# Performance work log

Hardware: AMD Instinct MI355X
Metric: run time of the kernel (lower is better)

The kernel has to match this reference:

```python
import jax, jax.numpy as jnp
import numpy as np

D_MODEL = 1024
D_FF = 2048
N_EXPERTS = 4
TOP_K = 2
INIT_STD = 0.02


def setup_inputs() -> dict:
    key = jax.random.key(0)
    ks = jax.random.split(key, 5)
    hidden_states = jax.random.normal(ks[0], (2, 2048, D_MODEL), dtype=jnp.float32)
    # gate: nn.Linear(d_model, num_experts, bias=False) -> weight [E, D]
    w_gate = jax.random.normal(ks[1], (N_EXPERTS, D_MODEL), dtype=jnp.float32) * INIT_STD
    # per-expert GLU MLP weights, stacked over the expert axis
    w_gate_proj = jax.random.normal(ks[2], (N_EXPERTS, D_MODEL, D_FF), dtype=jnp.float32) * INIT_STD
    w_up_proj = jax.random.normal(ks[3], (N_EXPERTS, D_MODEL, D_FF), dtype=jnp.float32) * INIT_STD
    w_down_proj = jax.random.normal(ks[4], (N_EXPERTS, D_FF, D_MODEL), dtype=jnp.float32) * INIT_STD
    return {
        "hidden_states": hidden_states,
        "w_gate": w_gate,
        "w_gate_proj": w_gate_proj,
        "w_up_proj": w_up_proj,
        "w_down_proj": w_down_proj,
    }


def reference(hidden_states, w_gate, w_gate_proj, w_up_proj, w_down_proj):
    B, S, D = hidden_states.shape
    x = hidden_states.reshape(-1, D)  # [T, D]
    # --- routing ---
    router_logits = x @ w_gate.T  # [T, E]
    routing_probs = jax.nn.softmax(router_logits.astype(jnp.float32), axis=-1)
    topw, sel = jax.lax.top_k(routing_probs, TOP_K)  # [T, K]
    topw = topw / jnp.sum(topw, axis=-1, keepdims=True)  # norm_topk_prob=True
    topw = topw.astype(x.dtype)
    # combine weights per (token, expert): zero for non-selected experts
    cw = jnp.sum(jax.nn.one_hot(sel, N_EXPERTS, dtype=x.dtype) * topw[..., None], axis=1)  # [T, E]
    # --- expert GLU MLPs (dense over experts, masked combine) ---
    g = jnp.einsum('td,edf->etf', x, w_gate_proj)  # [E, T, F]
    u = jnp.einsum('td,edf->etf', x, w_up_proj)
    h = jax.nn.gelu(g, approximate=False) * u  # torch F.gelu default = exact erf
    y = jnp.einsum('etf,efd->etd', h, w_down_proj)  # [E, T, D]
    out = jnp.einsum('etd,te->td', y, cw)  # weighted scatter-combine
    # dropout p=0.0 (eval) -> identity
    return out.reshape(B, S, D)
```

## Files before the change

### kernel.cpp

```cpp
#include <hip/hip_runtime.h>
#include <hip/hip_bf16.h>
#include <math.h>


typedef float  f32x4 __attribute__((ext_vector_type(4)));
typedef short  s16x8 __attribute__((ext_vector_type(8)));

__device__ __forceinline__ unsigned short f2bf(float f) {
  union { float f; unsigned int u; } v; v.f = f;
  return (unsigned short)((v.u + 0x7fffu + ((v.u >> 16) & 1u)) >> 16);
}

__device__ __forceinline__ void glds16(const void* g, void* l) {
  __builtin_amdgcn_global_load_lds(
      (const __attribute__((address_space(1))) void*)g,
      (__attribute__((address_space(3))) void*)l, 16, 0, 0);
}

__global__ void k_routing(const float* __restrict__ x, const float* __restrict__ wg,
                          float* __restrict__ cw, int* __restrict__ idx,
                          int* __restrict__ cnt, unsigned short* __restrict__ Xb) {
  const int lane = threadIdx.x & 63;
  const int tok  = blockIdx.x * 4 + (threadIdx.x >> 6);
  const float4* X4 = (const float4*)x + (size_t)tok * 256;
  const float4* W4 = (const float4*)wg;
  ushort4* O4 = (ushort4*)Xb + (size_t)tok * 256;
  float a0 = 0.f, a1 = 0.f, a2 = 0.f, a3 = 0.f;
#pragma unroll
  for (int j = 0; j < 4; ++j) {
    const int d4 = j * 64 + lane;
    const float4 v = X4[d4];
    ushort4 o;
    o.x = f2bf(v.x); o.y = f2bf(v.y); o.z = f2bf(v.z); o.w = f2bf(v.w);
    O4[d4] = o;
    float4 w;
    w = W4[0 * 256 + d4]; a0 += v.x * w.x + v.y * w.y + v.z * w.z + v.w * w.w;
    w = W4[1 * 256 + d4]; a1 += v.x * w.x + v.y * w.y + v.z * w.z + v.w * w.w;
    w = W4[2 * 256 + d4]; a2 += v.x * w.x + v.y * w.y + v.z * w.z + v.w * w.w;
    w = W4[3 * 256 + d4]; a3 += v.x * w.x + v.y * w.y + v.z * w.z + v.w * w.w;
  }
#pragma unroll
  for (int off = 32; off; off >>= 1) {
    a0 += __shfl_xor(a0, off);
    a1 += __shfl_xor(a1, off);
    a2 += __shfl_xor(a2, off);
    a3 += __shfl_xor(a3, off);
  }
  if (lane == 0) {
    float l[4] = {a0, a1, a2, a3};
    const float m = fmaxf(fmaxf(l[0], l[1]), fmaxf(l[2], l[3]));
    float p[4];
#pragma unroll
    for (int e = 0; e < 4; ++e) p[e] = expf(l[e] - m);
    int i1 = 0; float b1 = p[0];
#pragma unroll
    for (int e = 1; e < 4; ++e) if (p[e] > b1) { b1 = p[e]; i1 = e; }
    int i2 = -1; float b2 = -1.f;
#pragma unroll
    for (int e = 0; e < 4; ++e) if (e != i1 && p[e] > b2) { b2 = p[e]; i2 = e; }
    const float inv = 1.f / (b1 + b2);
    float o[4] = {0.f, 0.f, 0.f, 0.f};
    o[i1] = b1 * inv; o[i2] = b2 * inv;
    *(float4*)(cw + (size_t)tok * 4) = make_float4(o[0], o[1], o[2], o[3]);
    const int p1 = atomicAdd(&cnt[i1], 1); idx[i1 * 4096 + p1] = tok;
    const int p2 = atomicAdd(&cnt[i2], 1); idx[i2 * 4096 + p2] = tok;
  }
}

__global__ void k_offsets(const int* __restrict__ cnt, int* __restrict__ off) {
  if (threadIdx.x == 0 && blockIdx.x == 0) {
    int o = 0, q = 0, p = 0;
#pragma unroll
    for (int e = 0; e < 4; ++e) {
      off[e] = o; off[4 + e] = q; off[9 + e] = p;
      o += (cnt[e] + 255) & ~255;
      q += (cnt[e] + 255) >> 8;
      p += (cnt[e] + 127) >> 7;
    }
    off[8] = q; off[13] = p;
  }
}

__global__ void k_tcvt_all(const float* __restrict__ wgp, const float* __restrict__ wup,
                           const float* __restrict__ wdp,
                           unsigned short* __restrict__ Wcat,
                           unsigned short* __restrict__ Wdt) {
  __shared__ float t[64][65];
  const int z = blockIdx.z;
  const int tx = threadIdx.x, ty = threadIdx.y;
  const float* in; unsigned short* outp; int R, C, c0, r0, cat = 0, addup = 0;
  if (z < 8) {
    R = 1024; C = 2048;
    const int e = z & 3;
    in   = (z < 4 ? wgp : wup) + (size_t)e * 1024 * 2048;
    outp = Wcat + (size_t)e * 4096 * 1024;
    c0 = blockIdx.x * 64; r0 = blockIdx.y * 64;
    cat = 1; addup = (z >= 4) ? 16 : 0;
  } else {
    R = 2048; C = 1024;
    const int e = z & 3;
    in   = wdp + (size_t)e * 2048 * 1024;
    outp = Wdt + (size_t)e * 2048 * 1024;
    c0 = blockIdx.y * 64; r0 = blockIdx.x * 64;
  }
#pragma unroll
  for (int i = 0; i < 16; ++i) {
    const int r = i * 4 + ty;
    t[r][tx] = in[(size_t)(r0 + r) * C + c0 + tx];
  }
  __syncthreads();
#pragma unroll
  for (int i = 0; i < 16; ++i) {
    const int cc = i * 4 + ty;
    const int f = c0 + cc;
    const int orow = cat ? (((f >> 4) << 5) + (f & 15) + addup) : f;
    outp[(size_t)orow * R + r0 + tx] = f2bf(t[tx][cc]);
  }
}

__global__ __launch_bounds__(512, 2)
void k_gemm1(const unsigned short* __restrict__ Xb,
             const unsigned short* __restrict__ Wcat,
             unsigned short* __restrict__ H,
             const int* __restrict__ idx, const int* __restrict__ cnt,
             const int* __restrict__ off) {
  const int w0 = (blockIdx.x & 7) * 72 + (blockIdx.x >> 3);
  const int bn = w0 / 36, mt = w0 % 36;
  const int* t1 = off + 4;
  if (mt >= t1[4]) return;
  const int e = (mt >= t1[1]) + (mt >= t1[2]) + (mt >= t1[3]);
  const int local = mt - t1[e];
  const int cn = cnt[e];
  const int lr0 = local * 256;
  const int hrow0 = off[e] + lr0;

  __shared__ __align__(16) unsigned short lds[2][2][256 * 64];

  const int tid = threadIdx.x;
  const int lane = tid & 63, wv = tid >> 6;
  const int wm = wv >> 2, wn = wv & 3;
  const int l15 = lane & 15;
  const int kb0 = ((lane >> 4) * 16) ^ ((lane & 7) << 4);
  const int kb1 = kb0 ^ 64;
  const int lrow = lane >> 3;
  const int scol = ((lane & 7) ^ lrow) * 8;
  const int wbase = wv * 8;

  int tk[4];
#pragma unroll
  for (int j = 0; j < 4; ++j)
    tk[j] = idx[e * 4096 + min(lr0 + j * 64 + wbase + lrow, cn - 1)];

  const unsigned short* Wb = Wcat + (size_t)e * 4096 * 1024 + (size_t)(bn * 256) * 1024;

  f32x4 acc[8][4] = {};

#pragma unroll
  for (int j = 0; j < 4; ++j)
    glds16(Xb + (size_t)tk[j] * 1024 + scol, &lds[0][0][(j * 64 + wbase) * 64]);
#pragma unroll
  for (int j = 0; j < 4; ++j)
    glds16(Wb + (size_t)(j * 64 + wbase + lrow) * 1024 + scol, &lds[0][1][(j * 64 + wbase) * 64]);

  for (int kt = 0; kt < 16; ++kt) {
    const int cur = kt & 1;
    asm volatile("s_waitcnt vmcnt(0)" ::: "memory");
    asm volatile("s_barrier" ::: "memory");
    if (kt < 15) {
      const int ko = (kt + 1) * 64;
#pragma unroll
      for (int j = 0; j < 4; ++j)
        glds16(Xb + (size_t)tk[j] * 1024 + ko + scol, &lds[cur ^ 1][0][(j * 64 + wbase) * 64]);
#pragma unroll
      for (int j = 0; j < 4; ++j)
        glds16(Wb + (size_t)(j * 64 + wbase + lrow) * 1024 + ko + scol, &lds[cur ^ 1][1][(j * 64 + wbase) * 64]);
    }
    const char* Ab = (const char*)lds[cur][0];
    const char* Bb = (const char*)lds[cur][1];
    s16x8 bfr[4][2];
#pragma unroll
    for (int ni = 0; ni < 4; ++ni) {
      const int row = wn * 64 + ni * 16 + l15;
      bfr[ni][0] = *(const s16x8*)(Bb + row * 128 + kb0);
      bfr[ni][1] = *(const s16x8*)(Bb + row * 128 + kb1);
    }
#pragma unroll
    for (int p = 0; p < 4; ++p) {
      const int r0a = wm * 128 + (2 * p) * 16 + l15;
      const int r1a = wm * 128 + (2 * p + 1) * 16 + l15;
      const s16x8 a0k0 = *(const s16x8*)(Ab + r0a * 128 + kb0);
      const s16x8 a0k1 = *(const s16x8*)(Ab + r0a * 128 + kb1);
      const s16x8 a1k0 = *(const s16x8*)(Ab + r1a * 128 + kb0);
      const s16x8 a1k1 = *(const s16x8*)(Ab + r1a * 128 + kb1);
      __builtin_amdgcn_s_setprio(1);
#pragma unroll
      for (int ni = 0; ni < 4; ++ni) {
        acc[2 * p][ni]     = __builtin_amdgcn_mfma_f32_16x16x32_bf16(a0k0, bfr[ni][0], acc[2 * p][ni], 0, 0, 0);
        acc[2 * p][ni]     = __builtin_amdgcn_mfma_f32_16x16x32_bf16(a0k1, bfr[ni][1], acc[2 * p][ni], 0, 0, 0);
        acc[2 * p + 1][ni] = __builtin_amdgcn_mfma_f32_16x16x32_bf16(a1k0, bfr[ni][0], acc[2 * p + 1][ni], 0, 0, 0);
        acc[2 * p + 1][ni] = __builtin_amdgcn_mfma_f32_16x16x32_bf16(a1k1, bfr[ni][1], acc[2 * p + 1][ni], 0, 0, 0);
      }
      __builtin_amdgcn_s_setprio(0);
    }
  }

  const int rbase = hrow0 + wm * 128;
#pragma unroll
  for (int mi = 0; mi < 8; ++mi)
#pragma unroll
    for (int q = 0; q < 2; ++q)
#pragma unroll
      for (int r = 0; r < 4; ++r) {
        const int row = rbase + mi * 16 + (lane >> 4) * 4 + r;
        const int col = bn * 128 + wn * 32 + q * 16 + l15;
        const float g = acc[mi][2 * q][r];
        const float u = acc[mi][2 * q + 1][r];
        const float h = 0.5f * g * (1.0f + erff(g * 0.70710678118654752f)) * u;
        H[(size_t)row * 2048 + col] = f2bf(h);
      }
}

__global__ __launch_bounds__(256, 2)
void k_gemm2(const unsigned short* __restrict__ H,
             const unsigned short* __restrict__ Wdt,
             const float* __restrict__ cw,
             const int* __restrict__ idx, const int* __restrict__ cnt,
             const int* __restrict__ off,
             float* __restrict__ out) {
  const int w = (blockIdx.x & 7) * 68 + (blockIdx.x >> 3);
  const int mt = w >> 3, bn = w & 7;
  const int* t2 = off + 9;
  if (mt >= t2[4]) return;
  const int e = (mt >= t2[1]) + (mt >= t2[2]) + (mt >= t2[3]);
  const int local = mt - t2[e];
  const int cn = cnt[e];
  const int lr0 = local * 128;
  const int hrow0 = off[e] + lr0;

  __shared__ __align__(16) unsigned short lds[2][2][128 * 64];

  const int lane = threadIdx.x & 63, wid = threadIdx.x >> 6;
  const int wm = wid >> 1, wn = wid & 1;
  const int l15 = lane & 15;
  const int kb0 = ((lane >> 4) * 16) ^ ((lane & 7) << 4);
  const int kb1 = kb0 ^ 64;
  const int lrow = lane >> 3;
  const int scol = ((lane & 7) ^ lrow) * 8;
  const int wbase = wid * 8;

  const unsigned short* Ha = H + (size_t)hrow0 * 2048;
  const unsigned short* Wd = Wdt + (size_t)e * 1024 * 2048 + (size_t)(bn * 128) * 2048;

  f32x4 acc[4][4] = {};

#pragma unroll
  for (int j = 0; j < 4; ++j) {
    const int r = j * 32 + wbase;
    glds16(Ha + (size_t)(r + lrow) * 2048 + scol, &lds[0][0][r * 64]);
    glds16(Wd + (size_t)(r + lrow) * 2048 + scol, &lds[0][1][r * 64]);
  }

  for (int kt = 0; kt < 32; ++kt) {
    const int cur = kt & 1;
    asm volatile("s_waitcnt vmcnt(0)" ::: "memory");
    asm volatile("s_barrier" ::: "memory");
    if (kt < 31) {
      const int ko = (kt + 1) * 64;
#pragma unroll
      for (int j = 0; j < 4; ++j) {
        const int r = j * 32 + wbase;
        glds16(Ha + (size_t)(r + lrow) * 2048 + ko + scol, &lds[cur ^ 1][0][r * 64]);
        glds16(Wd + (size_t)(r + lrow) * 2048 + ko + scol, &lds[cur ^ 1][1][r * 64]);
      }
    }
    const char* Ab = (const char*)lds[cur][0];
    const char* Bb = (const char*)lds[cur][1];
    s16x8 bfr[4][2];
#pragma unroll
    for (int ni = 0; ni < 4; ++ni) {
      const int row = wn * 64 + ni * 16 + l15;
      bfr[ni][0] = *(const s16x8*)(Bb + row * 128 + kb0);
      bfr[ni][1] = *(const s16x8*)(Bb + row * 128 + kb1);
    }
#pragma unroll
    for (int mi = 0; mi < 4; ++mi) {
      const int ra = wm * 64 + mi * 16 + l15;
      const s16x8 ak0 = *(const s16x8*)(Ab + ra * 128 + kb0);
      const s16x8 ak1 = *(const s16x8*)(Ab + ra * 128 + kb1);
      __builtin_amdgcn_s_setprio(1);
#pragma unroll
      for (int ni = 0; ni < 4; ++ni) {
        acc[mi][ni] = __builtin_amdgcn_mfma_f32_16x16x32_bf16(ak0, bfr[ni][0], acc[mi][ni], 0, 0, 0);
        acc[mi][ni] = __builtin_amdgcn_mfma_f32_16x16x32_bf16(ak1, bfr[ni][1], acc[mi][ni], 0, 0, 0);
      }
      __builtin_amdgcn_s_setprio(0);
    }
  }

#pragma unroll
  for (int mi = 0; mi < 4; ++mi)
#pragma unroll
    for (int r = 0; r < 4; ++r) {
      const int lr = lr0 + wm * 64 + mi * 16 + (lane >> 4) * 4 + r;
      if (lr < cn) {
        const int tok = idx[e * 4096 + lr];
        const float wgt = cw[(size_t)tok * 4 + e];
        float* orow = out + (size_t)tok * 1024 + bn * 128 + wn * 64 + l15;
#pragma unroll
        for (int ni = 0; ni < 4; ++ni)
          atomicAdd(orow + ni * 16, acc[mi][ni][r] * wgt);
      }
    }
}

extern "C" void kernel_launch(void* const* d_in, const int* in_sizes, int n_in,
                              void* d_out, int out_size, void* d_ws, size_t ws_size,
                              hipStream_t stream) {
  const float* x     = (const float*)d_in[0];
  const float* wgate = (const float*)d_in[1];
  const float* wgp   = (const float*)d_in[2];
  const float* wup   = (const float*)d_in[3];
  const float* wdp   = (const float*)d_in[4];
  float* out = (float*)d_out;

  char* ws = (char*)d_ws;
  float* cw            = (float*)ws;
  int*   idx           = (int*)(ws + 65536);
  int*   cnt           = (int*)(ws + 131072);
  int*   off           = (int*)(ws + 131136);
  unsigned short* Xb   = (unsigned short*)(ws + 131584);
  unsigned short* Wcat = Xb   + (size_t)4096 * 1024;
  unsigned short* Wdt  = Wcat + (size_t)4 * 4096 * 1024;
  unsigned short* H    = Wdt  + (size_t)4 * 1024 * 2048;

  hipMemsetAsync(cnt, 0, 16, stream);
  hipMemsetAsync(out, 0, (size_t)4096 * 1024 * 4, stream);
  k_routing<<<1024, 256, 0, stream>>>(x, wgate, cw, idx, cnt, Xb);
  k_offsets<<<1, 64, 0, stream>>>(cnt, off);
  k_tcvt_all<<<dim3(32, 16, 12), dim3(64, 4), 0, stream>>>(wgp, wup, wdp, Wcat, Wdt);

  k_gemm1<<<576, 512, 0, stream>>>(Xb, Wcat, H, idx, cnt, off);
  k_gemm2<<<544, 256, 0, stream>>>(H, Wdt, cw, idx, cnt, off, out);
}
```

Before: 315.2 us.

## Replace atomic scatter-add epilogue with bf16 expert outputs and gather-combine kernel

The down-projection GEMM now writes its per-expert results as bf16 rows into a scratch buffer, which reuses the no-longer-needed activation/weight staging area, instead of atomically adding weighted fp32 values into the output. Routing records each token's two (expert, slot) positions. A new combine kernel then gathers the two rows per token, applies the routing weights and writes the output once. This removes the output memset and the contended global float atomics, at the cost of an extra kernel launch, an extra bf16 round trip through memory, and an added bf16 rounding of expert outputs before combining.

```diff
diff --git a/kernel.cpp b/kernel.cpp
--- a/kernel.cpp
+++ b/kernel.cpp
@@ -9,6 +9,10 @@
 __device__ __forceinline__ unsigned short f2bf(float f) {
   union { float f; unsigned int u; } v; v.f = f;
   return (unsigned short)((v.u + 0x7fffu + ((v.u >> 16) & 1u)) >> 16);
+}
+__device__ __forceinline__ float bf2f(unsigned short b) {
+  union { unsigned int u; float f; } v; v.u = ((unsigned int)b) << 16;
+  return v.f;
 }
 
 __device__ __forceinline__ void glds16(const void* g, void* l) {
@@ -19,7 +23,8 @@
 
 __global__ void k_routing(const float* __restrict__ x, const float* __restrict__ wg,
                           float* __restrict__ cw, int* __restrict__ idx,
-                          int* __restrict__ cnt, unsigned short* __restrict__ Xb) {
+                          int* __restrict__ cnt, unsigned short* __restrict__ Xb,
+                          int4* __restrict__ pos) {
   const int lane = threadIdx.x & 63;
   const int tok  = blockIdx.x * 4 + (threadIdx.x >> 6);
   const float4* X4 = (const float4*)x + (size_t)tok * 256;
@@ -64,6 +69,7 @@
     *(float4*)(cw + (size_t)tok * 4) = make_float4(o[0], o[1], o[2], o[3]);
     const int p1 = atomicAdd(&cnt[i1], 1); idx[i1 * 4096 + p1] = tok;
     const int p2 = atomicAdd(&cnt[i2], 1); idx[i2 * 4096 + p2] = tok;
+    pos[tok] = make_int4(i1, p1, i2, p2);
   }
 }
 
@@ -223,17 +229,14 @@
 __global__ __launch_bounds__(256, 2)
 void k_gemm2(const unsigned short* __restrict__ H,
              const unsigned short* __restrict__ Wdt,
-             const float* __restrict__ cw,
-             const int* __restrict__ idx, const int* __restrict__ cnt,
-             const int* __restrict__ off,
-             float* __restrict__ out) {
+             const int* __restrict__ cnt, const int* __restrict__ off,
+             unsigned short* __restrict__ Y) {
   const int w = (blockIdx.x & 7) * 68 + (blockIdx.x >> 3);
   const int mt = w >> 3, bn = w & 7;
   const int* t2 = off + 9;
   if (mt >= t2[4]) return;
   const int e = (mt >= t2[1]) + (mt >= t2[2]) + (mt >= t2[3]);
   const int local = mt - t2[e];
-  const int cn = cnt[e];
   const int lr0 = local * 128;
   const int hrow0 = off[e] + lr0;
 
@@ -297,20 +300,39 @@
     }
   }
 
+  const int rbase = hrow0 + wm * 64;
 #pragma unroll
   for (int mi = 0; mi < 4; ++mi)
 #pragma unroll
     for (int r = 0; r < 4; ++r) {
-      const int lr = lr0 + wm * 64 + mi * 16 + (lane >> 4) * 4 + r;
-      if (lr < cn) {
-        const int tok = idx[e * 4096 + lr];
-        const float wgt = cw[(size_t)tok * 4 + e];
-        float* orow = out + (size_t)tok * 1024 + bn * 128 + wn * 64 + l15;
-#pragma unroll
-        for (int ni = 0; ni < 4; ++ni)
-          atomicAdd(orow + ni * 16, acc[mi][ni][r] * wgt);
-      }
-    }
+      const int row = rbase + mi * 16 + (lane >> 4) * 4 + r;
+      unsigned short* yrow = Y + (size_t)row * 1024 + bn * 128 + wn * 64 + l15;
+#pragma unroll
+      for (int ni = 0; ni < 4; ++ni)
+        yrow[ni * 16] = f2bf(acc[mi][ni][r]);
+    }
+}
+
+__global__ void k_combine(const unsigned short* __restrict__ Y,
+                          const int4* __restrict__ pos,
+                          const float* __restrict__ cw,
+                          const int* __restrict__ off,
+                          float* __restrict__ out) {
+  const int tok = blockIdx.x;
+  const int d4 = threadIdx.x;
+  const int4 p = pos[tok];
+  const int r1 = off[p.x] + p.y;
+  const int r2 = off[p.z] + p.w;
+  const float w1 = cw[(size_t)tok * 4 + p.x];
+  const float w2 = cw[(size_t)tok * 4 + p.z];
+  const ushort4 y1 = ((const ushort4*)(Y + (size_t)r1 * 1024))[d4];
+  const ushort4 y2 = ((const ushort4*)(Y + (size_t)r2 * 1024))[d4];
+  float4 o;
+  o.x = w1 * bf2f(y1.x) + w2 * bf2f(y2.x);
+  o.y = w1 * bf2f(y1.y) + w2 * bf2f(y2.y);
+  o.z = w1 * bf2f(y1.z) + w2 * bf2f(y2.z);
+  o.w = w1 * bf2f(y1.w) + w2 * bf2f(y2.w);
+  ((float4*)(out + (size_t)tok * 1024))[d4] = o;
 }
 
 extern "C" void kernel_launch(void* const* d_in, const int* in_sizes, int n_in,
@@ -326,19 +348,21 @@
   char* ws = (char*)d_ws;
   float* cw            = (float*)ws;
   int*   idx           = (int*)(ws + 65536);
-  int*   cnt           = (int*)(ws + 131072);
-  int*   off           = (int*)(ws + 131136);
-  unsigned short* Xb   = (unsigned short*)(ws + 131584);
+  int4*  pos           = (int4*)(ws + 131072);
+  int*   cnt           = (int*)(ws + 196608);
+  int*   off           = (int*)(ws + 196672);
+  unsigned short* Xb   = (unsigned short*)(ws + 262144);
   unsigned short* Wcat = Xb   + (size_t)4096 * 1024;
   unsigned short* Wdt  = Wcat + (size_t)4 * 4096 * 1024;
   unsigned short* H    = Wdt  + (size_t)4 * 1024 * 2048;
+  unsigned short* Y    = Xb;
 
   hipMemsetAsync(cnt, 0, 16, stream);
-  hipMemsetAsync(out, 0, (size_t)4096 * 1024 * 4, stream);
-  k_routing<<<1024, 256, 0, stream>>>(x, wgate, cw, idx, cnt, Xb);
+  k_routing<<<1024, 256, 0, stream>>>(x, wgate, cw, idx, cnt, Xb, pos);
   k_offsets<<<1, 64, 0, stream>>>(cnt, off);
   k_tcvt_all<<<dim3(32, 16, 12), dim3(64, 4), 0, stream>>>(wgp, wup, wdp, Wcat, Wdt);
 
   k_gemm1<<<576, 512, 0, stream>>>(Xb, Wcat, H, idx, cnt, off);
-  k_gemm2<<<544, 256, 0, stream>>>(H, Wdt, cw, idx, cnt, off, out);
-}
+  k_gemm2<<<544, 256, 0, stream>>>(H, Wdt, cnt, off, Y);
+  k_combine<<<4096, 256, 0, stream>>>(Y, pos, cw, off, out);
+}
```

Result: faster. 293.3 us (-6.9%).
